# Performance work log

Hardware: AMD Instinct MI355X
Metric: run time of the kernel (lower is better)

Reference implementation:

```python
import jax, jax.numpy as jnp
import numpy as np

N_EMBD = 768
N_EXPERTS = 8
TOP_K = 2
D_FF = 4 * N_EMBD


def setup_inputs() -> dict:
    key = jax.random.key(0)
    k1, k2, k3, k4 = jax.random.split(key, 4)
    x = jax.random.normal(k1, (2, 2048, N_EMBD), dtype=jnp.float32)
    gate_w = jax.random.normal(k2, (N_EMBD, N_EXPERTS), dtype=jnp.float32) * (1.0 / np.sqrt(N_EMBD))
    w_fc = jax.random.normal(k3, (N_EXPERTS, N_EMBD, D_FF), dtype=jnp.float32) * (1.0 / np.sqrt(N_EMBD))
    w_proj = jax.random.normal(k4, (N_EXPERTS, D_FF, N_EMBD), dtype=jnp.float32) * (1.0 / np.sqrt(D_FF))
    return {"x": x, "gate_w": gate_w, "w_fc": w_fc, "w_proj": w_proj}


def reference(x, gate_w, w_fc, w_proj):
    B, S, D = x.shape
    E = w_fc.shape[0]
    xt = x.reshape(-1, D)                    # [T, D]
    T = xt.shape[0]
    scores = xt @ gate_w                      # [T, E]
    expert_weights, expert_indices = jax.lax.top_k(scores, TOP_K)  # [T, K]
    expert_weights = jax.nn.softmax(expert_weights, axis=-1)
    # per-token combine weight for each expert (0 if expert not selected)
    comb = jnp.zeros((T, E), dtype=xt.dtype)
    comb = comb.at[jnp.arange(T)[:, None], expert_indices].add(expert_weights)  # [T, E]
    out = jnp.zeros_like(xt)
    for e in range(E):  # fixed small loop over experts
        h = jax.nn.gelu(xt @ w_fc[e], approximate=False)  # torch nn.GELU default = exact erf
        y_e = h @ w_proj[e]                               # [T, D]
        out = out + comb[:, e:e + 1] * y_e
    return out.reshape(B, S, D)
```

## Files before the change

### kernel.cpp

```cpp
#include <hip/hip_runtime.h>
#include <hip/hip_bf16.h>
#include <math.h>

#define T_TOK 4096
#define D_EMB 768
#define DFF   3072
#define N_EXP 8
#define MAXT  72
#define CNTS  16

typedef __attribute__((ext_vector_type(8))) short bf16x8;
typedef __attribute__((ext_vector_type(4))) float f32x4;

typedef __attribute__((address_space(3))) unsigned int lds_u32_t;
typedef __attribute__((address_space(1))) unsigned int glob_u32_t;

__device__ __forceinline__ void gload16(const void* g, void* l) {
  __builtin_amdgcn_global_load_lds((const glob_u32_t*)g, (lds_u32_t*)l, 16, 0, 0);
}

__device__ __forceinline__ short f2bf(float f) {
  union { __hip_bfloat16 b; short s; } u;
  u.b = __float2bfloat16(f);
  return u.s;
}

__global__ void zero_init_kernel(float4* __restrict__ out4, int n4, int* __restrict__ cnt) {
  int i = blockIdx.x * blockDim.x + threadIdx.x;
  if (i < N_EXP * CNTS) cnt[i] = 0;
  float4 z; z.x = z.y = z.z = z.w = 0.f;
  for (int j = i; j < n4; j += gridDim.x * blockDim.x) out4[j] = z;
}

__global__ void cast_x_kernel(const float4* __restrict__ in, short4* __restrict__ outp, int n4) {
  int i = blockIdx.x * blockDim.x + threadIdx.x;
  if (i >= n4) return;
  float4 v = in[i];
  short4 o;
  o.x = f2bf(v.x); o.y = f2bf(v.y); o.z = f2bf(v.z); o.w = f2bf(v.w);
  outp[i] = o;
}

__global__ void transpose_cast_kernel(const float* __restrict__ in, short* __restrict__ outp,
                                      int R, int C) {
  __shared__ float tile[64][65];
  int e = blockIdx.z;
  int c0 = blockIdx.x * 64, r0 = blockIdx.y * 64;
  const float* src = in + (size_t)e * R * C;
  short* dst = outp + (size_t)e * R * C;
  int tid = threadIdx.x;
#pragma unroll
  for (int it = 0; it < 4; ++it) {
    int idx = tid + it * 256;
    int r = idx >> 4;
    int c4 = idx & 15;
    float4 v = *(const float4*)&src[(size_t)(r0 + r) * C + c0 + c4 * 4];
    tile[r][c4 * 4 + 0] = v.x; tile[r][c4 * 4 + 1] = v.y;
    tile[r][c4 * 4 + 2] = v.z; tile[r][c4 * 4 + 3] = v.w;
  }
  __syncthreads();
#pragma unroll
  for (int it = 0; it < 4; ++it) {
    int idx = tid + it * 256;
    int c = idx >> 4;
    int rr = idx & 15;
    short4 o;
    o.x = f2bf(tile[rr * 4 + 0][c]);
    o.y = f2bf(tile[rr * 4 + 1][c]);
    o.z = f2bf(tile[rr * 4 + 2][c]);
    o.w = f2bf(tile[rr * 4 + 3][c]);
    *(short4*)&dst[(size_t)(c0 + c) * R + r0 + rr * 4] = o;
  }
}

__global__ __launch_bounds__(256)
void gate_kernel(const float* __restrict__ x, const float* __restrict__ gw,
                 int* __restrict__ cnt, int* __restrict__ tok,
                 float* __restrict__ wgt) {
  __shared__ int lcnt[N_EXP];
  __shared__ int gbase[N_EXP];
  __shared__ int le[32];
  __shared__ float lw[32];
  __shared__ int lpos[32];
  int tid = threadIdx.x, lane = tid & 63, wid = tid >> 6;
  if (tid < N_EXP) lcnt[tid] = 0;
  __syncthreads();

#pragma unroll
  for (int i = 0; i < 4; i++) {
    int t = blockIdx.x * 16 + wid * 4 + i;
    float s[N_EXP];
#pragma unroll
    for (int e = 0; e < N_EXP; e++) s[e] = 0.f;
#pragma unroll
    for (int dd = 0; dd < D_EMB / 64; dd++) {
      int d = dd * 64 + lane;
      float xv = x[(size_t)t * D_EMB + d];
#pragma unroll
      for (int e = 0; e < N_EXP; e++) s[e] += xv * gw[d * N_EXP + e];
    }
#pragma unroll
    for (int e = 0; e < N_EXP; e++) {
#pragma unroll
      for (int off = 32; off > 0; off >>= 1) s[e] += __shfl_xor(s[e], off, 64);
    }
    if (lane == 0) {
      int e0 = 0;
#pragma unroll
      for (int e = 1; e < N_EXP; e++) if (s[e] > s[e0]) e0 = e;
      int e1 = -1;
#pragma unroll
      for (int e = 0; e < N_EXP; e++) {
        if (e == e0) continue;
        if (e1 < 0 || s[e] > s[e1]) e1 = e;
      }
      float p1 = __expf(s[e1] - s[e0]);
      float inv = 1.f / (1.f + p1);
      int idx = (wid * 4 + i) * 2;
      le[idx] = e0; lw[idx] = inv;           lpos[idx] = atomicAdd(&lcnt[e0], 1);
      le[idx + 1] = e1; lw[idx + 1] = p1 * inv; lpos[idx + 1] = atomicAdd(&lcnt[e1], 1);
    }
  }
  __syncthreads();
  if (tid < N_EXP) gbase[tid] = atomicAdd(&cnt[tid * CNTS], lcnt[tid]);
  __syncthreads();
  if (tid < 32) {
    int e = le[tid];
    int t = blockIdx.x * 16 + (tid >> 1);
    int p = gbase[e] + lpos[tid];
    tok[e * T_TOK + p] = t;
    wgt[e * T_TOK + p] = lw[tid];
  }
}

__global__ void plan_kernel(const int* __restrict__ cnt, int* __restrict__ offs,
                            int* __restrict__ tile_e, int* __restrict__ tile_rt,
                            int* __restrict__ ntiles) {
  if (threadIdx.x != 0 || blockIdx.x != 0) return;
  int o = 0, nt = 0;
  for (int e = 0; e < N_EXP; e++) {
    offs[e] = o;
    int tc = (cnt[e * CNTS] + 127) >> 7;
    for (int i = 0; i < tc; i++) { tile_e[nt] = e; tile_rt[nt] = i; nt++; }
    o += cnt[e * CNTS];
  }
  *ntiles = nt;
}

template<int KDIM, int NDIM, int EPI>
__global__ __launch_bounds__(256, 4)
void moe_gemm(const short* __restrict__ A, const short* __restrict__ Bw,
              const int* __restrict__ tok, const float* __restrict__ wgt,
              const int* __restrict__ cnt, const int* __restrict__ offs,
              const int* __restrict__ tile_e, const int* __restrict__ tile_rt,
              const int* __restrict__ ntiles,
              short* __restrict__ hout, float* __restrict__ fout) {
  const int COLT = NDIM / 128;
  int nwg = gridDim.x;
  int cpx = nwg >> 3;
  int logical = (blockIdx.x & 7) * cpx + (blockIdx.x >> 3);
  int tile = logical / COLT, ct = logical % COLT;
  if (tile >= *ntiles) return;
  int e = tile_e[tile], rt = tile_rt[tile];
  int ne = cnt[e * CNTS];
  int base = offs[e];

  __shared__ __align__(16) short As[2][128 * 32];
  __shared__ __align__(16) short Bs[2][128 * 32];

  int tid = threadIdx.x;
  int lane = tid & 63;
  int wid = tid >> 6;

  const short* aptr[2];
  const short* bptr[2];
  int lofs[2];
#pragma unroll
  for (int i = 0; i < 2; i++) {
    int seg = tid + i * 256;
    int row = seg >> 2;
    int p = seg & 3;
    int q = p ^ ((row ^ (row >> 2)) & 3);
    int r = rt * 128 + row;
    if (r >= ne) r = ne - 1;
    size_t ga = (EPI == 0) ? (size_t)tok[e * T_TOK + r] : (size_t)(base + r);
    aptr[i] = A + ga * KDIM + q * 8;
    bptr[i] = Bw + ((size_t)e * NDIM + ct * 128 + row) * KDIM + q * 8;
    lofs[i] = seg * 8;
  }

  f32x4 acc[4][4];
#pragma unroll
  for (int m = 0; m < 4; m++)
#pragma unroll
    for (int n = 0; n < 4; n++) acc[m][n] = (f32x4){0.f, 0.f, 0.f, 0.f};

  int wr = (wid >> 1) * 64, wc = (wid & 1) * 64;

#pragma unroll
  for (int i = 0; i < 2; i++) {
    gload16(aptr[i], &As[0][lofs[i]]);
    gload16(bptr[i], &Bs[0][lofs[i]]);
  }
  __syncthreads();

  const int NKT = KDIM / 32;
  int cur = 0;
  for (int kt = 0; kt < NKT; ++kt) {
    if (kt + 1 < NKT) {
      int k0 = (kt + 1) * 32;
#pragma unroll
      for (int i = 0; i < 2; i++) {
        gload16(aptr[i] + k0, &As[cur ^ 1][lofs[i]]);
        gload16(bptr[i] + k0, &Bs[cur ^ 1][lofs[i]]);
      }
    }
    int cb = lane >> 4;
    bf16x8 af[4], bv[4];
#pragma unroll
    for (int m = 0; m < 4; m++) {
      int row = wr + m * 16 + (lane & 15);
      af[m] = *(const bf16x8*)&As[cur][row * 32 + ((cb ^ ((row ^ (row >> 2)) & 3)) * 8)];
    }
#pragma unroll
    for (int n = 0; n < 4; n++) {
      int row = wc + n * 16 + (lane & 15);
      bv[n] = *(const bf16x8*)&Bs[cur][row * 32 + ((cb ^ ((row ^ (row >> 2)) & 3)) * 8)];
    }
#pragma unroll
    for (int m = 0; m < 4; m++)
#pragma unroll
      for (int n = 0; n < 4; n++)
        acc[m][n] = __builtin_amdgcn_mfma_f32_16x16x32_bf16(af[m], bv[n], acc[m][n], 0, 0, 0);
    __syncthreads();
    cur ^= 1;
  }

  int colbase = ct * 128 + wc;
#pragma unroll
  for (int m = 0; m < 4; m++) {
#pragma unroll
    for (int j = 0; j < 4; j++) {
      int rloc = rt * 128 + wr + m * 16 + ((lane >> 4) << 2) + j;
      if (rloc < ne) {
        if (EPI == 0) {
          size_t hrow = (size_t)(base + rloc) * NDIM;
#pragma unroll
          for (int n = 0; n < 4; n++) {
            float v = acc[m][n][j];
            float g = 0.5f * v * (1.0f + erff(v * 0.70710678118f));
            hout[hrow + colbase + n * 16 + (lane & 15)] = f2bf(g);
          }
        } else {
          int t = tok[e * T_TOK + rloc];
          float w = wgt[e * T_TOK + rloc];
          float* orow = fout + (size_t)t * NDIM + colbase + (lane & 15);
#pragma unroll
          for (int n = 0; n < 4; n++)
            atomicAdd(orow + n * 16, w * acc[m][n][j]);
        }
      }
    }
  }
}

extern "C" void kernel_launch(void* const* d_in, const int* in_sizes, int n_in,
                              void* d_out, int out_size, void* d_ws, size_t ws_size,
                              hipStream_t stream) {
  const float* x   = (const float*)d_in[0];
  const float* gw  = (const float*)d_in[1];
  const float* wfc = (const float*)d_in[2];
  const float* wpj = (const float*)d_in[3];
  float* out = (float*)d_out;

  char* ws = (char*)d_ws;
  const size_t SZ_XB = (size_t)T_TOK * D_EMB * 2;
  const size_t SZ_W  = (size_t)N_EXP * D_EMB * DFF * 2;
  const size_t SZ_H  = (size_t)2 * T_TOK * DFF * 2;
  short* xb   = (short*)(ws);
  short* wfcT = (short*)(ws + SZ_XB);
  short* wpjT = (short*)(ws + SZ_XB + SZ_W);
  short* h    = (short*)(ws + SZ_XB + 2 * SZ_W);
  char* p2    = ws + SZ_XB + 2 * SZ_W + SZ_H;
  int*   tok  = (int*)(p2);
  float* wgt  = (float*)(p2 + (size_t)N_EXP * T_TOK * 4);
  char* p3    = p2 + (size_t)N_EXP * T_TOK * 8;
  int*   cnt     = (int*)(p3);
  int*   offs    = (int*)(p3 + 1024);
  int*   tile_e  = (int*)(p3 + 1024 + 64);
  int*   tile_rt = (int*)(p3 + 1024 + 64 + 512);
  int*   ntiles  = (int*)(p3 + 1024 + 64 + 1024);

  int n4 = out_size / 4;
  zero_init_kernel<<<2048, 256, 0, stream>>>((float4*)out, n4, cnt);
  cast_x_kernel<<<(T_TOK * D_EMB / 4 + 255) / 256, 256, 0, stream>>>(
      (const float4*)x, (short4*)xb, T_TOK * D_EMB / 4);
  transpose_cast_kernel<<<dim3(DFF / 64, D_EMB / 64, N_EXP), 256, 0, stream>>>(wfc, wfcT, D_EMB, DFF);
  transpose_cast_kernel<<<dim3(D_EMB / 64, DFF / 64, N_EXP), 256, 0, stream>>>(wpj, wpjT, DFF, D_EMB);
  gate_kernel<<<T_TOK / 16, 256, 0, stream>>>(x, gw, cnt, tok, wgt);
  plan_kernel<<<1, 1, 0, stream>>>(cnt, offs, tile_e, tile_rt, ntiles);
  moe_gemm<D_EMB, DFF, 0><<<MAXT * (DFF / 128), 256, 0, stream>>>(
      xb, wfcT, tok, wgt, cnt, offs, tile_e, tile_rt, ntiles, h, nullptr);
  moe_gemm<DFF, D_EMB, 1><<<MAXT * (D_EMB / 128), 256, 0, stream>>>(
      h, wpjT, tok, wgt, cnt, offs, tile_e, tile_rt, ntiles, nullptr, out);
}
```

Baseline: 237.1 us.

## Triple-buffer MoE GEMM LDS pipeline and split-K the down projection

Replaces the double-buffered k-loop with a three-stage LDS ring using explicit vmcnt waits and a single barrier per step, precomputing LDS fragment offsets. Adds a split-K template parameter and runs the down-projection GEMM with two K-splits, doubling its grid to improve CU occupancy. This relies on atomic accumulation into the zeroed output, adds extra atomic traffic, and lowers the launch-bounds occupancy hint to 3 because of the larger LDS footprint.

```diff
diff --git a/kernel.cpp b/kernel.cpp
--- a/kernel.cpp
+++ b/kernel.cpp
@@ -147,8 +147,8 @@
   *ntiles = nt;
 }
 
-template<int KDIM, int NDIM, int EPI>
-__global__ __launch_bounds__(256, 4)
+template<int KDIM, int NDIM, int SPLITK, int EPI>
+__global__ __launch_bounds__(256, 3)
 void moe_gemm(const short* __restrict__ A, const short* __restrict__ Bw,
               const int* __restrict__ tok, const float* __restrict__ wgt,
               const int* __restrict__ cnt, const int* __restrict__ offs,
@@ -156,37 +156,67 @@
               const int* __restrict__ ntiles,
               short* __restrict__ hout, float* __restrict__ fout) {
   const int COLT = NDIM / 128;
+  const int KS = KDIM / SPLITK;
+  const int NKT = KS / 32;
+  static_assert(NKT % 3 == 0 && NKT >= 6, "pipeline needs NKT%3==0");
+
   int nwg = gridDim.x;
   int cpx = nwg >> 3;
   int logical = (blockIdx.x & 7) * cpx + (blockIdx.x >> 3);
-  int tile = logical / COLT, ct = logical % COLT;
+  int ct = logical % COLT;
+  int tile = (logical / COLT) % MAXT;
+  int sk = logical / (COLT * MAXT);
   if (tile >= *ntiles) return;
   int e = tile_e[tile], rt = tile_rt[tile];
   int ne = cnt[e * CNTS];
   int base = offs[e];
 
-  __shared__ __align__(16) short As[2][128 * 32];
-  __shared__ __align__(16) short Bs[2][128 * 32];
+  __shared__ __align__(16) short LDS[3 * 2 * 4096];
+  short* A0 = LDS;              short* B0 = LDS + 4096;
+  short* A1 = LDS + 2 * 4096;   short* B1 = LDS + 3 * 4096;
+  short* A2 = LDS + 4 * 4096;   short* B2 = LDS + 5 * 4096;
 
   int tid = threadIdx.x;
   int lane = tid & 63;
   int wid = tid >> 6;
 
-  const short* aptr[2];
-  const short* bptr[2];
-  int lofs[2];
-#pragma unroll
-  for (int i = 0; i < 2; i++) {
-    int seg = tid + i * 256;
-    int row = seg >> 2;
-    int p = seg & 3;
+  const short* aptr0; const short* aptr1;
+  const short* bptr0; const short* bptr1;
+  int lofs0, lofs1;
+  {
+    int seg = tid;
+    int row = seg >> 2, p = seg & 3;
     int q = p ^ ((row ^ (row >> 2)) & 3);
-    int r = rt * 128 + row;
-    if (r >= ne) r = ne - 1;
+    int r = rt * 128 + row; if (r >= ne) r = ne - 1;
     size_t ga = (EPI == 0) ? (size_t)tok[e * T_TOK + r] : (size_t)(base + r);
-    aptr[i] = A + ga * KDIM + q * 8;
-    bptr[i] = Bw + ((size_t)e * NDIM + ct * 128 + row) * KDIM + q * 8;
-    lofs[i] = seg * 8;
+    aptr0 = A + ga * KDIM + sk * KS + q * 8;
+    bptr0 = Bw + ((size_t)e * NDIM + ct * 128 + row) * KDIM + sk * KS + q * 8;
+    lofs0 = seg * 8;
+  }
+  {
+    int seg = tid + 256;
+    int row = seg >> 2, p = seg & 3;
+    int q = p ^ ((row ^ (row >> 2)) & 3);
+    int r = rt * 128 + row; if (r >= ne) r = ne - 1;
+    size_t ga = (EPI == 0) ? (size_t)tok[e * T_TOK + r] : (size_t)(base + r);
+    aptr1 = A + ga * KDIM + sk * KS + q * 8;
+    bptr1 = Bw + ((size_t)e * NDIM + ct * 128 + row) * KDIM + sk * KS + q * 8;
+    lofs1 = seg * 8;
+  }
+
+  int wr = (wid >> 1) * 64, wc = (wid & 1) * 64;
+  int cb = lane >> 4;
+
+  int offa[4], offb[4];
+#pragma unroll
+  for (int m = 0; m < 4; m++) {
+    int row = wr + m * 16 + (lane & 15);
+    offa[m] = row * 32 + (cb ^ ((row ^ (row >> 2)) & 3)) * 8;
+  }
+#pragma unroll
+  for (int n = 0; n < 4; n++) {
+    int row = wc + n * 16 + (lane & 15);
+    offb[n] = row * 32 + (cb ^ ((row ^ (row >> 2)) & 3)) * 8;
   }
 
   f32x4 acc[4][4];
@@ -195,46 +225,45 @@
 #pragma unroll
     for (int n = 0; n < 4; n++) acc[m][n] = (f32x4){0.f, 0.f, 0.f, 0.f};
 
-  int wr = (wid >> 1) * 64, wc = (wid & 1) * 64;
-
-#pragma unroll
-  for (int i = 0; i < 2; i++) {
-    gload16(aptr[i], &As[0][lofs[i]]);
-    gload16(bptr[i], &Bs[0][lofs[i]]);
-  }
-  __syncthreads();
-
-  const int NKT = KDIM / 32;
-  int cur = 0;
-  for (int kt = 0; kt < NKT; ++kt) {
-    if (kt + 1 < NKT) {
-      int k0 = (kt + 1) * 32;
-#pragma unroll
-      for (int i = 0; i < 2; i++) {
-        gload16(aptr[i] + k0, &As[cur ^ 1][lofs[i]]);
-        gload16(bptr[i] + k0, &Bs[cur ^ 1][lofs[i]]);
-      }
-    }
-    int cb = lane >> 4;
-    bf16x8 af[4], bv[4];
-#pragma unroll
-    for (int m = 0; m < 4; m++) {
-      int row = wr + m * 16 + (lane & 15);
-      af[m] = *(const bf16x8*)&As[cur][row * 32 + ((cb ^ ((row ^ (row >> 2)) & 3)) * 8)];
-    }
-#pragma unroll
-    for (int n = 0; n < 4; n++) {
-      int row = wc + n * 16 + (lane & 15);
-      bv[n] = *(const bf16x8*)&Bs[cur][row * 32 + ((cb ^ ((row ^ (row >> 2)) & 3)) * 8)];
-    }
-#pragma unroll
-    for (int m = 0; m < 4; m++)
-#pragma unroll
-      for (int n = 0; n < 4; n++)
-        acc[m][n] = __builtin_amdgcn_mfma_f32_16x16x32_bf16(af[m], bv[n], acc[m][n], 0, 0, 0);
-    __syncthreads();
-    cur ^= 1;
-  }
+  gload16(aptr0, A0 + lofs0); gload16(bptr0, B0 + lofs0);
+  gload16(aptr1, A0 + lofs1); gload16(bptr1, B0 + lofs1);
+  gload16(aptr0 + 32, A1 + lofs0); gload16(bptr0 + 32, B1 + lofs0);
+  gload16(aptr1 + 32, A1 + lofs1); gload16(bptr1 + 32, B1 + lofs1);
+
+#define VMW(N) do { asm volatile("s_waitcnt vmcnt(" #N ")" ::: "memory"); \
+                    __builtin_amdgcn_sched_barrier(0); } while (0)
+#define STEP(CA, CB, SA, SB, K0, DOSTAGE, WN) do {                          \
+    VMW(WN);                                                                \
+    __builtin_amdgcn_s_barrier();                                           \
+    if (DOSTAGE) {                                                          \
+      gload16(aptr0 + (K0), (SA) + lofs0);                                  \
+      gload16(bptr0 + (K0), (SB) + lofs0);                                  \
+      gload16(aptr1 + (K0), (SA) + lofs1);                                  \
+      gload16(bptr1 + (K0), (SB) + lofs1);                                  \
+    }                                                                       \
+    bf16x8 af_[4], bv_[4];                                                  \
+    _Pragma("unroll") for (int m_ = 0; m_ < 4; ++m_)                        \
+      af_[m_] = *(const bf16x8*)((CA) + offa[m_]);                          \
+    _Pragma("unroll") for (int n_ = 0; n_ < 4; ++n_)                        \
+      bv_[n_] = *(const bf16x8*)((CB) + offb[n_]);                          \
+    _Pragma("unroll") for (int m_ = 0; m_ < 4; ++m_)                        \
+      _Pragma("unroll") for (int n_ = 0; n_ < 4; ++n_)                      \
+        acc[m_][n_] = __builtin_amdgcn_mfma_f32_16x16x32_bf16(              \
+            af_[m_], bv_[n_], acc[m_][n_], 0, 0, 0);                        \
+  } while (0)
+
+  int kb = 64;
+  for (int j = 0; j < NKT / 3 - 1; ++j) {
+    STEP(A0, B0, A2, B2, kb,      true, 4);
+    STEP(A1, B1, A0, B0, kb + 32, true, 4);
+    STEP(A2, B2, A1, B1, kb + 64, true, 4);
+    kb += 96;
+  }
+  STEP(A0, B0, A2, B2, kb, true, 4);
+  STEP(A1, B1, A0, B0, 0, false, 4);
+  STEP(A2, B2, A1, B1, 0, false, 0);
+#undef STEP
+#undef VMW
 
   int colbase = ct * 128 + wc;
 #pragma unroll
@@ -299,8 +328,8 @@
   transpose_cast_kernel<<<dim3(D_EMB / 64, DFF / 64, N_EXP), 256, 0, stream>>>(wpj, wpjT, DFF, D_EMB);
   gate_kernel<<<T_TOK / 16, 256, 0, stream>>>(x, gw, cnt, tok, wgt);
   plan_kernel<<<1, 1, 0, stream>>>(cnt, offs, tile_e, tile_rt, ntiles);
-  moe_gemm<D_EMB, DFF, 0><<<MAXT * (DFF / 128), 256, 0, stream>>>(
+  moe_gemm<D_EMB, DFF, 1, 0><<<MAXT * (DFF / 128), 256, 0, stream>>>(
       xb, wfcT, tok, wgt, cnt, offs, tile_e, tile_rt, ntiles, h, nullptr);
-  moe_gemm<DFF, D_EMB, 1><<<MAXT * (D_EMB / 128), 256, 0, stream>>>(
+  moe_gemm<DFF, D_EMB, 2, 1><<<2 * MAXT * (D_EMB / 128), 256, 0, stream>>>(
       h, wpjT, tok, wgt, cnt, offs, tile_e, tile_rt, ntiles, nullptr, out);
 }
```

Result: no change. 233.6 us (-1.5%).

## Use 256x256 tiles with 1024-thread blocks and split-K for down projection

Applied to the files above, without the earlier changes.

Expert GEMM tiles grow from 128x128 with 256 threads to 256x256 with 1024 threads (16 waves), doubling reuse of each LDS tile per global load. The down-projection GEMM is split along K into two halves whose results are combined through the existing atomic adds, to restore parallelism lost by the larger tiles. LDS offset computation is hoisted out of the k-loop. Larger tiles cause more padding waste on partially filled expert tiles, and 64KB of LDS per block limits occupancy.

```diff
diff --git a/kernel.cpp b/kernel.cpp
--- a/kernel.cpp
+++ b/kernel.cpp
@@ -6,7 +6,7 @@
 #define D_EMB 768
 #define DFF   3072
 #define N_EXP 8
-#define MAXT  72
+#define MAXT2 40
 #define CNTS  16
 
 typedef __attribute__((ext_vector_type(8))) short bf16x8;
@@ -140,53 +140,71 @@
   int o = 0, nt = 0;
   for (int e = 0; e < N_EXP; e++) {
     offs[e] = o;
-    int tc = (cnt[e * CNTS] + 127) >> 7;
+    int tc = (cnt[e * CNTS] + 255) >> 8;
     for (int i = 0; i < tc; i++) { tile_e[nt] = e; tile_rt[nt] = i; nt++; }
     o += cnt[e * CNTS];
   }
   *ntiles = nt;
 }
 
-template<int KDIM, int NDIM, int EPI>
-__global__ __launch_bounds__(256, 4)
+template<int KDIM, int NDIM, int SPLITK, int EPI>
+__global__ __launch_bounds__(1024, 4)
 void moe_gemm(const short* __restrict__ A, const short* __restrict__ Bw,
               const int* __restrict__ tok, const float* __restrict__ wgt,
               const int* __restrict__ cnt, const int* __restrict__ offs,
               const int* __restrict__ tile_e, const int* __restrict__ tile_rt,
               const int* __restrict__ ntiles,
               short* __restrict__ hout, float* __restrict__ fout) {
-  const int COLT = NDIM / 128;
+  const int COLT = NDIM / 256;
+  const int KS = KDIM / SPLITK;
+  const int NKT = KS / 32;
+  static_assert(NKT >= 2, "need at least 2 k-steps");
+
   int nwg = gridDim.x;
   int cpx = nwg >> 3;
   int logical = (blockIdx.x & 7) * cpx + (blockIdx.x >> 3);
-  int tile = logical / COLT, ct = logical % COLT;
+  int ct = logical % COLT;
+  int tile = (logical / COLT) % MAXT2;
+  int sk = logical / (COLT * MAXT2);
   if (tile >= *ntiles) return;
   int e = tile_e[tile], rt = tile_rt[tile];
   int ne = cnt[e * CNTS];
   int base = offs[e];
 
-  __shared__ __align__(16) short As[2][128 * 32];
-  __shared__ __align__(16) short Bs[2][128 * 32];
+  __shared__ __align__(16) short As[2][256 * 32];
+  __shared__ __align__(16) short Bs[2][256 * 32];
 
   int tid = threadIdx.x;
   int lane = tid & 63;
   int wid = tid >> 6;
 
-  const short* aptr[2];
-  const short* bptr[2];
-  int lofs[2];
-#pragma unroll
-  for (int i = 0; i < 2; i++) {
-    int seg = tid + i * 256;
-    int row = seg >> 2;
-    int p = seg & 3;
+  const short* aptr;
+  const short* bptr;
+  int lofs;
+  {
+    int row = tid >> 2, p = tid & 3;
     int q = p ^ ((row ^ (row >> 2)) & 3);
-    int r = rt * 128 + row;
+    int r = rt * 256 + row;
     if (r >= ne) r = ne - 1;
     size_t ga = (EPI == 0) ? (size_t)tok[e * T_TOK + r] : (size_t)(base + r);
-    aptr[i] = A + ga * KDIM + q * 8;
-    bptr[i] = Bw + ((size_t)e * NDIM + ct * 128 + row) * KDIM + q * 8;
-    lofs[i] = seg * 8;
+    aptr = A + ga * KDIM + sk * KS + q * 8;
+    bptr = Bw + ((size_t)e * NDIM + ct * 256 + row) * KDIM + sk * KS + q * 8;
+    lofs = tid * 8;
+  }
+
+  int wr = (wid >> 2) * 64, wc = (wid & 3) * 64;
+  int cb = lane >> 4;
+
+  int offa[4], offb[4];
+#pragma unroll
+  for (int m = 0; m < 4; m++) {
+    int row = wr + m * 16 + (lane & 15);
+    offa[m] = row * 32 + (cb ^ ((row ^ (row >> 2)) & 3)) * 8;
+  }
+#pragma unroll
+  for (int n = 0; n < 4; n++) {
+    int row = wc + n * 16 + (lane & 15);
+    offb[n] = row * 32 + (cb ^ ((row ^ (row >> 2)) & 3)) * 8;
   }
 
   f32x4 acc[4][4];
@@ -195,38 +213,24 @@
 #pragma unroll
     for (int n = 0; n < 4; n++) acc[m][n] = (f32x4){0.f, 0.f, 0.f, 0.f};
 
-  int wr = (wid >> 1) * 64, wc = (wid & 1) * 64;
-
-#pragma unroll
-  for (int i = 0; i < 2; i++) {
-    gload16(aptr[i], &As[0][lofs[i]]);
-    gload16(bptr[i], &Bs[0][lofs[i]]);
-  }
-  __syncthreads();
-
-  const int NKT = KDIM / 32;
+  gload16(aptr, &As[0][lofs]);
+  gload16(bptr, &Bs[0][lofs]);
+  __syncthreads();
+
   int cur = 0;
   for (int kt = 0; kt < NKT; ++kt) {
     if (kt + 1 < NKT) {
       int k0 = (kt + 1) * 32;
-#pragma unroll
-      for (int i = 0; i < 2; i++) {
-        gload16(aptr[i] + k0, &As[cur ^ 1][lofs[i]]);
-        gload16(bptr[i] + k0, &Bs[cur ^ 1][lofs[i]]);
-      }
-    }
-    int cb = lane >> 4;
+      gload16(aptr + k0, &As[cur ^ 1][lofs]);
+      gload16(bptr + k0, &Bs[cur ^ 1][lofs]);
+    }
     bf16x8 af[4], bv[4];
 #pragma unroll
-    for (int m = 0; m < 4; m++) {
-      int row = wr + m * 16 + (lane & 15);
-      af[m] = *(const bf16x8*)&As[cur][row * 32 + ((cb ^ ((row ^ (row >> 2)) & 3)) * 8)];
-    }
-#pragma unroll
-    for (int n = 0; n < 4; n++) {
-      int row = wc + n * 16 + (lane & 15);
-      bv[n] = *(const bf16x8*)&Bs[cur][row * 32 + ((cb ^ ((row ^ (row >> 2)) & 3)) * 8)];
-    }
+    for (int m = 0; m < 4; m++)
+      af[m] = *(const bf16x8*)&As[cur][offa[m]];
+#pragma unroll
+    for (int n = 0; n < 4; n++)
+      bv[n] = *(const bf16x8*)&Bs[cur][offb[n]];
 #pragma unroll
     for (int m = 0; m < 4; m++)
 #pragma unroll
@@ -236,12 +240,12 @@
     cur ^= 1;
   }
 
-  int colbase = ct * 128 + wc;
+  int colbase = ct * 256 + wc;
 #pragma unroll
   for (int m = 0; m < 4; m++) {
 #pragma unroll
     for (int j = 0; j < 4; j++) {
-      int rloc = rt * 128 + wr + m * 16 + ((lane >> 4) << 2) + j;
+      int rloc = rt * 256 + wr + m * 16 + ((lane >> 4) << 2) + j;
       if (rloc < ne) {
         if (EPI == 0) {
           size_t hrow = (size_t)(base + rloc) * NDIM;
@@ -299,8 +303,8 @@
   transpose_cast_kernel<<<dim3(D_EMB / 64, DFF / 64, N_EXP), 256, 0, stream>>>(wpj, wpjT, DFF, D_EMB);
   gate_kernel<<<T_TOK / 16, 256, 0, stream>>>(x, gw, cnt, tok, wgt);
   plan_kernel<<<1, 1, 0, stream>>>(cnt, offs, tile_e, tile_rt, ntiles);
-  moe_gemm<D_EMB, DFF, 0><<<MAXT * (DFF / 128), 256, 0, stream>>>(
+  moe_gemm<D_EMB, DFF, 1, 0><<<MAXT2 * (DFF / 256), 1024, 0, stream>>>(
       xb, wfcT, tok, wgt, cnt, offs, tile_e, tile_rt, ntiles, h, nullptr);
-  moe_gemm<DFF, D_EMB, 1><<<MAXT * (D_EMB / 128), 256, 0, stream>>>(
+  moe_gemm<DFF, D_EMB, 2, 1><<<2 * MAXT2 * (D_EMB / 256), 1024, 0, stream>>>(
       h, wpjT, tok, wgt, cnt, offs, tile_e, tile_rt, ntiles, nullptr, out);
 }
```

Measured after the change: 244.7 us. 3.2% more time.
